# Kernel tuning notes

Measured on AMD Instinct MI355X. Metric: run time of the kernel, lower is better.

## Reference

```python
import jax, jax.numpy as jnp
import numpy as np
from jax.scipy.special import erf

N_POINTS = 4096
N_EVENTS = 1000000
BETA = 1.0   # init_beta, constant (not a Parameter in the torch module)
ALPHA = 1.0  # torch.ones((1,1)) buffer
WEIGHT = 1.0


def setup_inputs() -> dict:
    key = jax.random.key(0)
    k1, k2, k3, k4, k5 = jax.random.split(key, 5)
    return {
        "z0": jax.random.uniform(k1, (N_POINTS, 2), dtype=jnp.float32),
        "v0": jax.random.uniform(k2, (N_POINTS, 2), dtype=jnp.float32),
        "event_times": jax.random.uniform(k3, (N_EVENTS,), dtype=jnp.float32),
        "t0": jnp.zeros((), dtype=jnp.float32),
        "tn": jnp.ones((), dtype=jnp.float32),
        "u_idx": jax.random.randint(k4, (N_EVENTS,), 0, N_POINTS, dtype=jnp.int64) if jax.config.read('jax_enable_x64') else jax.random.randint(k4, (N_EVENTS,), 0, N_POINTS).astype(jnp.int32),
        "v_idx": jax.random.randint(k5, (N_EVENTS,), 0, N_POINTS).astype(jnp.int32),
    }


def reference(z0, v0, event_times, t0, tn, u_idx, v_idx):
    beta = jnp.float32(BETA)
    alpha = jnp.float32(ALPHA)

    # ---- event term: sum_e beta - ||z_u(t_e) - z_v(t_e)||^2,  z(t) = z0 + v0*t (a0 == 0)
    dz0 = z0[u_idx] - z0[v_idx]                      # [E, 2]
    dv0 = v0[u_idx] - v0[v_idx]                      # [E, 2]
    dz = dz0 + dv0 * event_times[:, None]            # [E, 2]
    d2 = jnp.sum(dz * dz, axis=-1)                   # [E]
    event_intensity = jnp.sum(beta - d2)

    # ---- non-event term: analytic Hawkes integral over all triu pairs
    i, j = jnp.triu_indices(z0.shape[0], k=1)        # static, [P]
    a = z0[i, 0] - z0[j, 0]
    b = z0[i, 1] - z0[j, 1]
    m = v0[i, 0] - v0[j, 0]
    n = v0[i, 1] - v0[j, 1]
    mn2 = m * m + n * n                              # [P]
    s = jnp.sqrt(alpha * mn2)
    cross = a * n - b * m
    dot = a * m + b * n
    expo = jnp.exp((-(cross * cross) * alpha + mn2 * beta) / mn2)
    sqrt_pi = jnp.float32(np.sqrt(np.pi))
    integral = (-sqrt_pi * expo
                * (erf(alpha * (mn2 * t0 + dot) / s) - erf(alpha * (mn2 * tn + dot) / s))
                / (2.0 * s))                          # [P]
    non_event_intensity = jnp.sum(integral)

    return event_intensity - WEIGHT * non_event_intensity
```

## Files before the change

### kernel.cpp

```cpp
#include <hip/hip_runtime.h>

#define NPTS   4096
#define NEVT   1000000
#define NQUAD  (NEVT / 4)
#define TILE   64
#define NT     (NPTS / TILE)
#define PAIR_BLOCKS (NT * (NT + 1) / 2)
#define BLK    1024
#define GRID   512
#define NWAVES (GRID * (BLK / 64))
#define NUNIT2 (PAIR_BLOCKS * 32)
#define PERW2  (NUNIT2 / NWAVES)
#define REMW2  (NUNIT2 % NWAVES)

#define LOG2E  1.4426950408889634f
#define EA1 0.278393f
#define EA2 0.230389f
#define EA3 0.000972f
#define EA4 0.078108f

__global__ __launch_bounds__(BLK, 8) void hawkes_fused(
    const float* __restrict__ z0, const float* __restrict__ v0,
    const float* __restrict__ et, const float* __restrict__ t0p,
    const float* __restrict__ tnp, const int* __restrict__ uix,
    const int* __restrict__ vix, float* __restrict__ out)
{
    __shared__ float4 pts[NPTS];
    __shared__ float  red[BLK / 64];
    const int tid = threadIdx.x;

    {
        const float4* z4 = (const float4*)z0;
        const float4* v4 = (const float4*)v0;
        #pragma unroll
        for (int k = 0; k < NPTS / (2 * BLK); ++k) {
            int p2 = tid + k * BLK;
            float4 zz = z4[p2];
            float4 vv = v4[p2];
            pts[2 * p2]     = make_float4(zz.x, zz.y, vv.x, vv.y);
            pts[2 * p2 + 1] = make_float4(zz.z, zz.w, vv.z, vv.w);
        }
    }
    __syncthreads();

    float acc_ev = 0.0f;
    {
        int ev0 = (int)(((long long)blockIdx.x * NQUAD) / GRID);
        int ev1 = (int)(((long long)(blockIdx.x + 1) * NQUAD) / GRID);
        int q = ev0 + tid;
        if (q < ev1) {
            int base = q * 4;
            float4 t4 = *(const float4*)(et + base);
            int4   u4 = *(const int4*)(uix + base);
            int4   v4 = *(const int4*)(vix + base);
            float tt[4] = {t4.x, t4.y, t4.z, t4.w};
            int   uu[4] = {u4.x, u4.y, u4.z, u4.w};
            int   vv[4] = {v4.x, v4.y, v4.z, v4.w};
            #pragma unroll
            for (int e = 0; e < 4; ++e) {
                float4 P = pts[uu[e]];
                float4 Q = pts[vv[e]];
                float dx = __builtin_fmaf(P.z - Q.z, tt[e], P.x - Q.x);
                float dy = __builtin_fmaf(P.w - Q.w, tt[e], P.y - Q.y);
                acc_ev += 1.0f - (dx * dx + dy * dy);
            }
        }
    }

    const float t0 = *t0p;
    const float tn = *tnp;
    const int il  = tid & 63;
    const int wid = (int)blockIdx.x * (BLK / 64) + (tid >> 6);
    int u    = wid * PERW2 + (wid < REMW2 ? wid : REMW2);
    int uend = u + PERW2 + (wid < REMW2 ? 1 : 0);
    float acc0 = 0.0f, acc1 = 0.0f;
    while (u < uend) {
        int L = u >> 5;
        int bi = (int)((129.0f - sqrtf((float)(16641 - 8 * L))) * 0.5f);
        while (bi * NT - bi * (bi - 1) / 2 > L) --bi;
        while ((bi + 1) * NT - (bi + 1) * bi / 2 <= L) ++bi;
        int bj = bi + (L - (bi * NT - bi * (bi - 1) / 2));
        int ibase = bi * TILE, jbase = bj * TILE;
        int i = ibase + il;
        float4 Pi = pts[i];
        int run_end = (L + 1) << 5;
        if (run_end > uend) run_end = uend;
        for (; u < run_end; ++u) {
            int j0 = jbase + ((u & 31) << 1);
            int j1 = j0 + 1;
            float4 tj0 = pts[j0];
            float4 tj1 = pts[j1];
            float a0 = Pi.x - tj0.x, a1 = Pi.x - tj1.x;
            float b0 = Pi.y - tj0.y, b1 = Pi.y - tj1.y;
            float m0 = Pi.z - tj0.z, m1 = Pi.z - tj1.z;
            float n0 = Pi.w - tj0.w, n1 = Pi.w - tj1.w;
            float mn0 = __builtin_fmaf(m0, m0, n0 * n0);
            float mn1 = __builtin_fmaf(m1, m1, n1 * n1);
            float cr0 = __builtin_fmaf(a0, n0, -b0 * m0);
            float cr1 = __builtin_fmaf(a1, n1, -b1 * m1);
            float dt0 = __builtin_fmaf(a0, m0, b0 * n0);
            float dt1 = __builtin_fmaf(a1, m1, b1 * n1);
            float is0 = __builtin_amdgcn_rsqf(mn0);
            float is1 = __builtin_amdgcn_rsqf(mn1);
            float g0  = cr0 * cr0 * (is0 * is0);
            float g1  = cr1 * cr1 * (is1 * is1);
            float e0  = __builtin_amdgcn_exp2f(__builtin_fmaf(-g0, LOG2E, LOG2E));
            float e1  = __builtin_amdgcn_exp2f(__builtin_fmaf(-g1, LOG2E, LOG2E));
            float A0  = __builtin_fmaf(mn0, t0, dt0) * is0;
            float B0  = __builtin_fmaf(mn0, tn, dt0) * is0;
            float A1  = __builtin_fmaf(mn1, t0, dt1) * is1;
            float B1  = __builtin_fmaf(mn1, tn, dt1) * is1;
            float xA0 = __builtin_fabsf(A0), xB0 = __builtin_fabsf(B0);
            float xA1 = __builtin_fabsf(A1), xB1 = __builtin_fabsf(B1);
            float PA0 = __builtin_fmaf(xA0, __builtin_fmaf(xA0, __builtin_fmaf(xA0,
                          __builtin_fmaf(xA0, EA4, EA3), EA2), EA1), 1.0f);
            float PB0 = __builtin_fmaf(xB0, __builtin_fmaf(xB0, __builtin_fmaf(xB0,
                          __builtin_fmaf(xB0, EA4, EA3), EA2), EA1), 1.0f);
            float PA1 = __builtin_fmaf(xA1, __builtin_fmaf(xA1, __builtin_fmaf(xA1,
                          __builtin_fmaf(xA1, EA4, EA3), EA2), EA1), 1.0f);
            float PB1 = __builtin_fmaf(xB1, __builtin_fmaf(xB1, __builtin_fmaf(xB1,
                          __builtin_fmaf(xB1, EA4, EA3), EA2), EA1), 1.0f);
            float R0  = __builtin_amdgcn_rcpf(PA0 * PB0);
            float R1  = __builtin_amdgcn_rcpf(PA1 * PB1);
            float rA0 = R0 * PB0, rB0 = R0 * PA0;
            float rA1 = R1 * PB1, rB1 = R1 * PA1;
            float qA0 = rA0 * rA0; qA0 *= qA0;
            float qB0 = rB0 * rB0; qB0 *= qB0;
            float qA1 = rA1 * rA1; qA1 *= qA1;
            float qB1 = rB1 * rB1; qB1 *= qB1;
            float eA0 = __builtin_copysignf(1.0f - qA0, A0);
            float eB0 = __builtin_copysignf(1.0f - qB0, B0);
            float eA1 = __builtin_copysignf(1.0f - qA1, A1);
            float eB1 = __builtin_copysignf(1.0f - qB1, B1);
            float t00 = (eB0 - eA0) * e0 * is0;
            float t11 = (eB1 - eA1) * e1 * is1;
            acc0 += (j0 > i) ? t00 : 0.0f;
            acc1 += (j1 > i) ? t11 : 0.0f;
        }
    }

    float contrib = __builtin_fmaf(-0.8862269254527580f, acc0 + acc1, acc_ev);

    #pragma unroll
    for (int off = 32; off > 0; off >>= 1)
        contrib += __shfl_down(contrib, off, 64);
    if ((tid & 63) == 0) red[tid >> 6] = contrib;
    __syncthreads();
    if (tid == 0) {
        float s = 0.0f;
        #pragma unroll
        for (int w = 0; w < BLK / 64; ++w) s += red[w];
        atomicAdd(out, s);
    }
}

extern "C" void kernel_launch(void* const* d_in, const int* in_sizes, int n_in,
                              void* d_out, int out_size, void* d_ws, size_t ws_size,
                              hipStream_t stream) {
    const float* z0  = (const float*)d_in[0];
    const float* v0  = (const float*)d_in[1];
    const float* et  = (const float*)d_in[2];
    const float* t0p = (const float*)d_in[3];
    const float* tnp = (const float*)d_in[4];
    const int*   uix = (const int*)d_in[5];
    const int*   vix = (const int*)d_in[6];
    float* out = (float*)d_out;

    hipLaunchKernelGGL(hawkes_fused, dim3(GRID), dim3(BLK), 0, stream,
                       z0, v0, et, t0p, tnp, uix, vix, out);
}
```

Baseline: 87.64 us.

## Switch shared points to SoA layout and vectorize pair math with packed float2

Stores the point table as four separate shared arrays instead of float4, so each pair iteration loads adjacent j0/j1 values as float2 per component. Rewrites the pair loop with two-wide float vector types so the compiler can emit packed FP32 instructions (v_pk_fma/mul/add) on CDNA3+. Sign transfer is done with bit masks, and launch bounds occupancy hint drops from 8 to 4. The separate-component gather may add LDS instructions in the event loop, and packed codegen depends on the compiler.

```diff
diff --git a/kernel.cpp b/kernel.cpp
--- a/kernel.cpp
+++ b/kernel.cpp
@@ -1,4 +1,7 @@
 #include <hip/hip_runtime.h>
+
+typedef float v2f __attribute__((ext_vector_type(2)));
+typedef unsigned int v2u __attribute__((ext_vector_type(2)));
 
 #define NPTS   4096
 #define NEVT   1000000
@@ -19,15 +22,32 @@
 #define EA3 0.000972f
 #define EA4 0.078108f
 
-__global__ __launch_bounds__(BLK, 8) void hawkes_fused(
+__device__ __forceinline__ v2f vabs2(v2f x) {
+    return (v2f){__builtin_fabsf(x.x), __builtin_fabsf(x.y)};
+}
+__device__ __forceinline__ v2f signed_one_minus(v2f q, v2f s) {
+    v2f r = (v2f){1.0f, 1.0f} - q;
+    v2u ru, su;
+    __builtin_memcpy(&ru, &r, 8);
+    __builtin_memcpy(&su, &s, 8);
+    ru |= (su & (v2u){0x80000000u, 0x80000000u});
+    v2f o;
+    __builtin_memcpy(&o, &ru, 8);
+    return o;
+}
+
+__global__ __launch_bounds__(BLK, 4) void hawkes_fused(
     const float* __restrict__ z0, const float* __restrict__ v0,
     const float* __restrict__ et, const float* __restrict__ t0p,
     const float* __restrict__ tnp, const int* __restrict__ uix,
     const int* __restrict__ vix, float* __restrict__ out)
 {
-    __shared__ float4 pts[NPTS];
-    __shared__ float  red[BLK / 64];
+    __shared__ float sx[NPTS], sy[NPTS], sz[NPTS], sw[NPTS];
+    __shared__ float red[BLK / 64];
     const int tid = threadIdx.x;
+
+    const float t0 = *t0p;
+    const float tn = *tnp;
 
     {
         const float4* z4 = (const float4*)z0;
@@ -37,8 +57,10 @@
             int p2 = tid + k * BLK;
             float4 zz = z4[p2];
             float4 vv = v4[p2];
-            pts[2 * p2]     = make_float4(zz.x, zz.y, vv.x, vv.y);
-            pts[2 * p2 + 1] = make_float4(zz.z, zz.w, vv.z, vv.w);
+            sx[2 * p2] = zz.x; sx[2 * p2 + 1] = zz.z;
+            sy[2 * p2] = zz.y; sy[2 * p2 + 1] = zz.w;
+            sz[2 * p2] = vv.x; sz[2 * p2 + 1] = vv.z;
+            sw[2 * p2] = vv.y; sw[2 * p2 + 1] = vv.w;
         }
     }
     __syncthreads();
@@ -58,22 +80,22 @@
             int   vv[4] = {v4.x, v4.y, v4.z, v4.w};
             #pragma unroll
             for (int e = 0; e < 4; ++e) {
-                float4 P = pts[uu[e]];
-                float4 Q = pts[vv[e]];
-                float dx = __builtin_fmaf(P.z - Q.z, tt[e], P.x - Q.x);
-                float dy = __builtin_fmaf(P.w - Q.w, tt[e], P.y - Q.y);
+                int a = uu[e], b = vv[e];
+                float dx = __builtin_fmaf(sz[a] - sz[b], tt[e], sx[a] - sx[b]);
+                float dy = __builtin_fmaf(sw[a] - sw[b], tt[e], sy[a] - sy[b]);
                 acc_ev += 1.0f - (dx * dx + dy * dy);
             }
         }
     }
 
-    const float t0 = *t0p;
-    const float tn = *tnp;
+    const v2f t0v = (v2f){t0, t0};
+    const v2f tnv = (v2f){tn, tn};
+    const v2f l2e = (v2f){LOG2E, LOG2E};
     const int il  = tid & 63;
     const int wid = (int)blockIdx.x * (BLK / 64) + (tid >> 6);
     int u    = wid * PERW2 + (wid < REMW2 ? wid : REMW2);
     int uend = u + PERW2 + (wid < REMW2 ? 1 : 0);
-    float acc0 = 0.0f, acc1 = 0.0f;
+    v2f accp = (v2f){0.0f, 0.0f};
     while (u < uend) {
         int L = u >> 5;
         int bi = (int)((129.0f - sqrtf((float)(16641 - 8 * L))) * 0.5f);
@@ -82,64 +104,54 @@
         int bj = bi + (L - (bi * NT - bi * (bi - 1) / 2));
         int ibase = bi * TILE, jbase = bj * TILE;
         int i = ibase + il;
-        float4 Pi = pts[i];
+        v2f pix = (v2f){sx[i], sx[i]};
+        v2f piy = (v2f){sy[i], sy[i]};
+        v2f piz = (v2f){sz[i], sz[i]};
+        v2f piw = (v2f){sw[i], sw[i]};
         int run_end = (L + 1) << 5;
         if (run_end > uend) run_end = uend;
         for (; u < run_end; ++u) {
             int j0 = jbase + ((u & 31) << 1);
-            int j1 = j0 + 1;
-            float4 tj0 = pts[j0];
-            float4 tj1 = pts[j1];
-            float a0 = Pi.x - tj0.x, a1 = Pi.x - tj1.x;
-            float b0 = Pi.y - tj0.y, b1 = Pi.y - tj1.y;
-            float m0 = Pi.z - tj0.z, m1 = Pi.z - tj1.z;
-            float n0 = Pi.w - tj0.w, n1 = Pi.w - tj1.w;
-            float mn0 = __builtin_fmaf(m0, m0, n0 * n0);
-            float mn1 = __builtin_fmaf(m1, m1, n1 * n1);
-            float cr0 = __builtin_fmaf(a0, n0, -b0 * m0);
-            float cr1 = __builtin_fmaf(a1, n1, -b1 * m1);
-            float dt0 = __builtin_fmaf(a0, m0, b0 * n0);
-            float dt1 = __builtin_fmaf(a1, m1, b1 * n1);
-            float is0 = __builtin_amdgcn_rsqf(mn0);
-            float is1 = __builtin_amdgcn_rsqf(mn1);
-            float g0  = cr0 * cr0 * (is0 * is0);
-            float g1  = cr1 * cr1 * (is1 * is1);
-            float e0  = __builtin_amdgcn_exp2f(__builtin_fmaf(-g0, LOG2E, LOG2E));
-            float e1  = __builtin_amdgcn_exp2f(__builtin_fmaf(-g1, LOG2E, LOG2E));
-            float A0  = __builtin_fmaf(mn0, t0, dt0) * is0;
-            float B0  = __builtin_fmaf(mn0, tn, dt0) * is0;
-            float A1  = __builtin_fmaf(mn1, t0, dt1) * is1;
-            float B1  = __builtin_fmaf(mn1, tn, dt1) * is1;
-            float xA0 = __builtin_fabsf(A0), xB0 = __builtin_fabsf(B0);
-            float xA1 = __builtin_fabsf(A1), xB1 = __builtin_fabsf(B1);
-            float PA0 = __builtin_fmaf(xA0, __builtin_fmaf(xA0, __builtin_fmaf(xA0,
-                          __builtin_fmaf(xA0, EA4, EA3), EA2), EA1), 1.0f);
-            float PB0 = __builtin_fmaf(xB0, __builtin_fmaf(xB0, __builtin_fmaf(xB0,
-                          __builtin_fmaf(xB0, EA4, EA3), EA2), EA1), 1.0f);
-            float PA1 = __builtin_fmaf(xA1, __builtin_fmaf(xA1, __builtin_fmaf(xA1,
-                          __builtin_fmaf(xA1, EA4, EA3), EA2), EA1), 1.0f);
-            float PB1 = __builtin_fmaf(xB1, __builtin_fmaf(xB1, __builtin_fmaf(xB1,
-                          __builtin_fmaf(xB1, EA4, EA3), EA2), EA1), 1.0f);
-            float R0  = __builtin_amdgcn_rcpf(PA0 * PB0);
-            float R1  = __builtin_amdgcn_rcpf(PA1 * PB1);
-            float rA0 = R0 * PB0, rB0 = R0 * PA0;
-            float rA1 = R1 * PB1, rB1 = R1 * PA1;
-            float qA0 = rA0 * rA0; qA0 *= qA0;
-            float qB0 = rB0 * rB0; qB0 *= qB0;
-            float qA1 = rA1 * rA1; qA1 *= qA1;
-            float qB1 = rB1 * rB1; qB1 *= qB1;
-            float eA0 = __builtin_copysignf(1.0f - qA0, A0);
-            float eB0 = __builtin_copysignf(1.0f - qB0, B0);
-            float eA1 = __builtin_copysignf(1.0f - qA1, A1);
-            float eB1 = __builtin_copysignf(1.0f - qB1, B1);
-            float t00 = (eB0 - eA0) * e0 * is0;
-            float t11 = (eB1 - eA1) * e1 * is1;
-            acc0 += (j0 > i) ? t00 : 0.0f;
-            acc1 += (j1 > i) ? t11 : 0.0f;
+            v2f tjx = *(const v2f*)&sx[j0];
+            v2f tjy = *(const v2f*)&sy[j0];
+            v2f tjz = *(const v2f*)&sz[j0];
+            v2f tjw = *(const v2f*)&sw[j0];
+            v2f a  = pix - tjx;
+            v2f b  = piy - tjy;
+            v2f m  = piz - tjz;
+            v2f n  = piw - tjw;
+            v2f mn2 = m * m + n * n;
+            v2f cr  = a * n - b * m;
+            v2f dt  = a * m + b * n;
+            v2f invs = (v2f){__builtin_amdgcn_rsqf(mn2.x),
+                             __builtin_amdgcn_rsqf(mn2.y)};
+            v2f g   = cr * cr * (invs * invs);
+            v2f exv = l2e - g * l2e;
+            v2f ee  = (v2f){__builtin_amdgcn_exp2f(exv.x),
+                            __builtin_amdgcn_exp2f(exv.y)};
+            v2f A   = (mn2 * t0v + dt) * invs;
+            v2f B   = (mn2 * tnv + dt) * invs;
+            v2f xA  = vabs2(A), xB = vabs2(B);
+            v2f PA  = (v2f){1.0f,1.0f} + xA*((v2f){EA1,EA1} + xA*((v2f){EA2,EA2}
+                        + xA*((v2f){EA3,EA3} + xA*(v2f){EA4,EA4})));
+            v2f PB  = (v2f){1.0f,1.0f} + xB*((v2f){EA1,EA1} + xB*((v2f){EA2,EA2}
+                        + xB*((v2f){EA3,EA3} + xB*(v2f){EA4,EA4})));
+            v2f PP  = PA * PB;
+            v2f R   = (v2f){__builtin_amdgcn_rcpf(PP.x),
+                            __builtin_amdgcn_rcpf(PP.y)};
+            v2f rA  = R * PB, rB = R * PA;
+            v2f qA  = rA * rA; qA *= qA;
+            v2f qB  = rB * rB; qB *= qB;
+            v2f eA  = signed_one_minus(qA, A);
+            v2f eB  = signed_one_minus(qB, B);
+            v2f term = (eB - eA) * ee * invs;
+            v2f sel = (v2f){ (j0     > i) ? term.x : 0.0f,
+                             (j0 + 1 > i) ? term.y : 0.0f };
+            accp += sel;
         }
     }
 
-    float contrib = __builtin_fmaf(-0.8862269254527580f, acc0 + acc1, acc_ev);
+    float contrib = __builtin_fmaf(-0.8862269254527580f, accp.x + accp.y, acc_ev);
 
     #pragma unroll
     for (int off = 32; off > 0; off >>= 1)
```

New measurement: 87.26 us. Within noise of the previous version (-0.4%).
